# Kernel optimization log

Measured on AMD Instinct MI355X. Metric: run time of the kernel, lower is better.

Reference implementation:

```python
import jax, jax.numpy as jnp
import numpy as np

H = 768        # hidden_size
NH = 12        # num_attention_heads
HD = H // NH   # head dim = 64
FF = 4 * H     # intermediate_size = 3072
EPS = 1e-12


def setup_inputs() -> dict:
    key = jax.random.key(0)
    ks = jax.random.split(key, 16)
    s = 0.02
    return {
        "hidden_state": jax.random.normal(ks[0], (16, 512, H), dtype=jnp.float32),
        "Wq": jax.random.normal(ks[1], (H, H), dtype=jnp.float32) * s,
        "bq": jnp.zeros((H,), jnp.float32),
        "Wk": jax.random.normal(ks[2], (H, H), dtype=jnp.float32) * s,
        "bk": jnp.zeros((H,), jnp.float32),
        "Wv": jax.random.normal(ks[3], (H, H), dtype=jnp.float32) * s,
        "bv": jnp.zeros((H,), jnp.float32),
        "Wo": jax.random.normal(ks[4], (H, H), dtype=jnp.float32) * s,
        "bo": jnp.zeros((H,), jnp.float32),
        "ln1_g": jnp.ones((H,), jnp.float32),
        "ln1_b": jnp.zeros((H,), jnp.float32),
        "W1": jax.random.normal(ks[5], (H, FF), dtype=jnp.float32) * s,
        "b1": jnp.zeros((FF,), jnp.float32),
        "W2": jax.random.normal(ks[6], (FF, H), dtype=jnp.float32) * s,
        "b2": jnp.zeros((H,), jnp.float32),
        "ln2_g": jnp.ones((H,), jnp.float32),
        "ln2_b": jnp.zeros((H,), jnp.float32),
    }


def _layer_norm(x, g, b):
    mu = jnp.mean(x, axis=-1, keepdims=True)
    var = jnp.mean(jnp.square(x - mu), axis=-1, keepdims=True)
    return (x - mu) * jax.lax.rsqrt(var + EPS) * g + b


def _split_heads(x):  # [b,s,H] -> [b,nh,s,hd]
    b, s, _ = x.shape
    return x.reshape(b, s, NH, HD).transpose(0, 2, 1, 3)


def reference(hidden_state, Wq, bq, Wk, bk, Wv, bv, Wo, bo,
              ln1_g, ln1_b, W1, b1, W2, b2, ln2_g, ln2_b):
    x = hidden_state
    b, s, _ = x.shape
    q = _split_heads(x @ Wq + bq)
    k = _split_heads(x @ Wk + bk)
    v = _split_heads(x @ Wv + bv)
    score = jnp.einsum("bhqd,bhkd->bhqk", q, k) / jnp.sqrt(jnp.float32(HD))
    score = jax.nn.softmax(score, axis=-1)  # dropout = identity (eval mode)
    ctx = jnp.einsum("bhqk,bhkd->bhqd", score, v)
    ctx = ctx.transpose(0, 2, 1, 3).reshape(b, s, H)
    attn_out = ctx @ Wo + bo
    h = _layer_norm(attn_out + x, ln1_g, ln1_b)
    ffn = jax.nn.gelu(h @ W1 + b1, approximate=False) @ W2 + b2
    return _layer_norm(ffn + h, ln2_g, ln2_b)
```

## Files before the change

### kernel.cpp

```cpp
#include <hip/hip_runtime.h>

typedef short short8 __attribute__((ext_vector_type(8)));
typedef float floatx4 __attribute__((ext_vector_type(4)));
typedef unsigned short u16;
typedef unsigned int u32;

__device__ __forceinline__ float bits2f(u16 u) {
  union { unsigned int i; float f; } w;
  w.i = ((unsigned int)u) << 16;
  return w.f;
}

__device__ __forceinline__ u16 f2bf(float f) {
  union { float f; unsigned int i; } w;
  w.f = f;
  unsigned int x = w.i;
  unsigned int r = (x + 0x7FFFu + ((x >> 16) & 1u)) >> 16;
  return (u16)r;
}

__device__ __forceinline__ void g2l16(const u16* g, u16* l) {
  __builtin_amdgcn_global_load_lds(
      (const __attribute__((address_space(1))) u32*)(const void*)g,
      (__attribute__((address_space(3))) u32*)(void*)l, 16, 0, 0);
}

__global__ __launch_bounds__(256) void prep_kernel(
    const float* __restrict__ x, u16* __restrict__ xb,
    const float* __restrict__ bq, const float* __restrict__ bk,
    const float* __restrict__ bv, float* __restrict__ biasqkv,
    const float* __restrict__ Wq, const float* __restrict__ Wk,
    const float* __restrict__ Wv, const float* __restrict__ Wo,
    const float* __restrict__ W1,
    u16* __restrict__ WTqkv, u16* __restrict__ WTo, u16* __restrict__ WT1) {
  __shared__ float tile[32][33];
  int bid = blockIdx.x;
  int tid = threadIdx.x;
  if (bid < 3072) {
    int i = bid * 256 + tid;
    const float4* p = (const float4*)x + (size_t)i * 2;
    float4 a = p[0], b = p[1];
    u16 t[8] = {f2bf(a.x), f2bf(a.y), f2bf(a.z), f2bf(a.w),
                f2bf(b.x), f2bf(b.y), f2bf(b.z), f2bf(b.w)};
    *(int4*)(xb + (size_t)i * 8) = *(const int4*)t;
    return;
  }
  if (bid < 3081) {
    int i = (bid - 3072) * 256 + tid;
    biasqkv[i] = (i < 768) ? bq[i] : (i < 1536 ? bk[i - 768] : bv[i - 1536]);
    return;
  }
  const float* W;
  u16* WT;
  int K, N, bx, by;
  if (bid < 5385) {
    int s = bid - 3081;
    int wsel = s / 576;
    int r = s - wsel * 576;
    K = 768; N = 768; bx = r % 24; by = r / 24;
    if (wsel == 0)      { W = Wq; WT = WTqkv; }
    else if (wsel == 1) { W = Wk; WT = WTqkv + 768 * 768; }
    else if (wsel == 2) { W = Wv; WT = WTqkv + 2 * 768 * 768; }
    else                { W = Wo; WT = WTo; }
  } else {
    int r = bid - 5385;
    K = 768; N = 3072; bx = r % 96; by = r / 96;
    W = W1; WT = WT1;
  }
  int tx = tid & 31, ty = tid >> 5;
  int n0 = bx * 32, k0 = by * 32;
#pragma unroll
  for (int i = 0; i < 4; i++)
    tile[ty + i * 8][tx] = W[(size_t)(k0 + ty + i * 8) * N + n0 + tx];
  __syncthreads();
#pragma unroll
  for (int i = 0; i < 4; i++)
    WT[(size_t)(n0 + ty + i * 8) * K + k0 + tx] = f2bf(tile[tx][ty + i * 8]);
}

__global__ __launch_bounds__(256) void transpose_k(const float* __restrict__ W,
                                                   u16* __restrict__ WT,
                                                   int K, int N) {
  __shared__ float tile[32][33];
  int tx = threadIdx.x & 31;
  int ty = threadIdx.x >> 5;
  int n0 = blockIdx.x * 32;
  int k0 = blockIdx.y * 32;
#pragma unroll
  for (int i = 0; i < 4; i++)
    tile[ty + i * 8][tx] = W[(size_t)(k0 + ty + i * 8) * N + n0 + tx];
  __syncthreads();
#pragma unroll
  for (int i = 0; i < 4; i++)
    WT[(size_t)(n0 + ty + i * 8) * K + k0 + tx] = f2bf(tile[tx][ty + i * 8]);
}

template <int BN>
__global__ __launch_bounds__(256) void gemm_m97(
    const u16* __restrict__ A, int lda, const u16* __restrict__ BT,
    const float* __restrict__ bias, void* __restrict__ Cv,
    int M, int N, int K, int act, int c_fp32) {
  constexpr int BM = 128, BK = 32;
  __shared__ __align__(16) u16 As[BM * BK];
  __shared__ __align__(16) u16 Bs[BN * BK];
  int tid = threadIdx.x;
  int wave = tid >> 6;
  int lane = tid & 63;
  int l15 = lane & 15;
  int quad = lane >> 4;

  int nb = gridDim.x;
  int lin = blockIdx.y * nb + blockIdx.x;
  int xcd = lin & 7;
  int i = lin >> 3;
  int grp = i / 48;
  int rem = i - grp * 48;
  int nblk = grp * 6 + (rem % 6);
  int mblk = (xcd << 3) + rem / 6;
  int m0 = mblk * BM;
  int n0 = nblk * BN;

  constexpr int MT = (BN == 128) ? 4 : 2;
  constexpr int NT = 4;
  int wm = (BN == 128) ? (wave & 1) * 64 : wave * 32;
  int wn = (BN == 128) ? (wave >> 1) * 64 : 0;

  floatx4 acc[MT][NT];
#pragma unroll
  for (int mi = 0; mi < MT; mi++)
#pragma unroll
    for (int ni = 0; ni < NT; ni++) acc[mi][ni] = (floatx4){0.f, 0.f, 0.f, 0.f};

  int srow = tid >> 2;
  int scol = (tid & 3) * 8;
  const u16* Ag0 = A + (size_t)(m0 + srow) * lda + scol;
  const u16* Ag1 = A + (size_t)(m0 + 64 + srow) * lda + scol;
  const u16* Bg0 = BT + (size_t)(n0 + srow) * K + scol;
  u16* AsW0 = As + wave * 512;
  u16* AsW1 = As + 2048 + wave * 512;
  u16* BsW0 = Bs + wave * 512;

  for (int k0 = 0; k0 < K; k0 += BK) {
    g2l16(Ag0 + k0, AsW0);
    g2l16(Ag1 + k0, AsW1);
    g2l16(Bg0 + k0, BsW0);
    if constexpr (BN == 128) {
      const u16* Bg1 = BT + (size_t)(n0 + 64 + srow) * K + scol;
      g2l16(Bg1 + k0, Bs + 2048 + wave * 512);
    }
    __syncthreads();
    short8 af[MT], bfr[NT];
#pragma unroll
    for (int mi = 0; mi < MT; mi++)
      af[mi] = *(const short8*)&As[(wm + mi * 16 + l15) * BK + quad * 8];
#pragma unroll
    for (int ni = 0; ni < NT; ni++)
      bfr[ni] = *(const short8*)&Bs[(wn + ni * 16 + l15) * BK + quad * 8];
#pragma unroll
    for (int mi = 0; mi < MT; mi++)
#pragma unroll
      for (int ni = 0; ni < NT; ni++)
        acc[mi][ni] = __builtin_amdgcn_mfma_f32_16x16x32_bf16(
            af[mi], bfr[ni], acc[mi][ni], 0, 0, 0);
    __syncthreads();
  }

#pragma unroll
  for (int mi = 0; mi < MT; mi++) {
#pragma unroll
    for (int ni = 0; ni < NT; ni++) {
      int col = n0 + wn + ni * 16 + l15;
      float bv = bias[col];
#pragma unroll
      for (int r = 0; r < 4; r++) {
        int row = m0 + wm + mi * 16 + quad * 4 + r;
        float v = acc[mi][ni][r] + bv;
        if (act == 1) v = 0.5f * v * (1.0f + erff(v * 0.70710678118654752f));
        if (c_fp32) ((float*)Cv)[(size_t)row * N + col] = v;
        else        ((u16*)Cv)[(size_t)row * N + col] = f2bf(v);
      }
    }
  }
}

__global__ __launch_bounds__(256) void attn_kernel(u16* __restrict__ qkv) {
  __shared__ __align__(16) u16 Qs[64][72];
  __shared__ __align__(16) u16 Ks[64][72];
  __shared__ __align__(16) u16 Vt[64][72];
  __shared__ __align__(16) u16 Ps[4][16][72];

  const int LD = 2304;
  int bh = blockIdx.x;
  int b = bh / 12;
  int h = bh - b * 12;
  int q0 = blockIdx.y * 64;
  size_t base = (size_t)b * 512 * LD + (size_t)h * 64;
  const u16* qg = qkv + base;
  const u16* kg = qkv + base + 768;
  const u16* vg = qkv + base + 1536;
  int tid = threadIdx.x;
  int wave = tid >> 6;
  int lane = tid & 63;
  int l15 = lane & 15;
  int quad = lane >> 4;

  int srow = tid >> 2;
  int sd = (tid & 3) * 16;

  {
    const u16* qp = qg + (size_t)(q0 + srow) * LD + sd;
    *(int4*)&Qs[srow][sd]     = *(const int4*)qp;
    *(int4*)&Qs[srow][sd + 8] = *(const int4*)(qp + 8);
  }
  __syncthreads();

  short8 aQ[2];
#pragma unroll
  for (int k = 0; k < 2; k++)
    aQ[k] = *(const short8*)&Qs[16 * wave + l15][k * 32 + quad * 8];

  floatx4 O[4];
  float m_r[4], l_r[4];
#pragma unroll
  for (int nt = 0; nt < 4; nt++) O[nt] = (floatx4){0.f, 0.f, 0.f, 0.f};
#pragma unroll
  for (int r = 0; r < 4; r++) { m_r[r] = -1e30f; l_r[r] = 0.f; }

  const float cst = 0.18033688011112042f;

  for (int c = 0; c < 8; c++) {
    const u16* kp = kg + (size_t)(c * 64 + srow) * LD + sd;
    const u16* vp = vg + (size_t)(c * 64 + srow) * LD + sd;
    int4 kv0 = *(const int4*)kp;
    int4 kv1 = *(const int4*)(kp + 8);
    int4 vv0 = *(const int4*)vp;
    int4 vv1 = *(const int4*)(vp + 8);
    __syncthreads();
    *(int4*)&Ks[srow][sd]     = kv0;
    *(int4*)&Ks[srow][sd + 8] = kv1;
    {
      u16 tv[16];
      *(int4*)tv = vv0;
      *(int4*)(tv + 8) = vv1;
#pragma unroll
      for (int j = 0; j < 16; j++) Vt[sd + j][srow] = tv[j];
    }
    __syncthreads();

    floatx4 S[4];
#pragma unroll
    for (int nt = 0; nt < 4; nt++) {
      floatx4 s = {0.f, 0.f, 0.f, 0.f};
      short8 bK0 = *(const short8*)&Ks[nt * 16 + l15][quad * 8];
      short8 bK1 = *(const short8*)&Ks[nt * 16 + l15][32 + quad * 8];
      s = __builtin_amdgcn_mfma_f32_16x16x32_bf16(aQ[0], bK0, s, 0, 0, 0);
      s = __builtin_amdgcn_mfma_f32_16x16x32_bf16(aQ[1], bK1, s, 0, 0, 0);
      S[nt] = s;
    }

#pragma unroll
    for (int r = 0; r < 4; r++) {
      float s0 = S[0][r] * cst, s1 = S[1][r] * cst;
      float s2 = S[2][r] * cst, s3 = S[3][r] * cst;
      float mr = fmaxf(fmaxf(s0, s1), fmaxf(s2, s3));
#pragma unroll
      for (int off = 1; off < 16; off <<= 1) mr = fmaxf(mr, __shfl_xor(mr, off, 16));
      float m_new = fmaxf(m_r[r], mr);
      float alpha = exp2f(m_r[r] - m_new);
      m_r[r] = m_new;
      float p0 = exp2f(s0 - m_new), p1 = exp2f(s1 - m_new);
      float p2 = exp2f(s2 - m_new), p3 = exp2f(s3 - m_new);
      S[0][r] = p0; S[1][r] = p1; S[2][r] = p2; S[3][r] = p3;
      float sum = p0 + p1 + p2 + p3;
#pragma unroll
      for (int off = 1; off < 16; off <<= 1) sum += __shfl_xor(sum, off, 16);
      l_r[r] = l_r[r] * alpha + sum;
      O[0][r] *= alpha; O[1][r] *= alpha; O[2][r] *= alpha; O[3][r] *= alpha;
    }

#pragma unroll
    for (int nt = 0; nt < 4; nt++)
#pragma unroll
      for (int r = 0; r < 4; r++)
        Ps[wave][quad * 4 + r][nt * 16 + l15] = f2bf(S[nt][r]);

    short8 aP[2];
#pragma unroll
    for (int k = 0; k < 2; k++)
      aP[k] = *(const short8*)&Ps[wave][l15][k * 32 + quad * 8];

#pragma unroll
    for (int nt = 0; nt < 4; nt++) {
      short8 bV0 = *(const short8*)&Vt[nt * 16 + l15][quad * 8];
      short8 bV1 = *(const short8*)&Vt[nt * 16 + l15][32 + quad * 8];
      O[nt] = __builtin_amdgcn_mfma_f32_16x16x32_bf16(aP[0], bV0, O[nt], 0, 0, 0);
      O[nt] = __builtin_amdgcn_mfma_f32_16x16x32_bf16(aP[1], bV1, O[nt], 0, 0, 0);
    }
  }

#pragma unroll
  for (int r = 0; r < 4; r++) {
    float inv = 1.0f / l_r[r];
    int row = q0 + 16 * wave + quad * 4 + r;
    u16* cp = qkv + base + (size_t)row * LD;
#pragma unroll
    for (int nt = 0; nt < 4; nt++)
      cp[nt * 16 + l15] = f2bf(O[nt][r] * inv);
  }
}

__global__ __launch_bounds__(256) void ln1_kernel(
    const u16* __restrict__ a, const float* __restrict__ r,
    const float* __restrict__ g, const float* __restrict__ bb,
    u16* __restrict__ out) {
  int row = blockIdx.x;
  int tid = threadIdx.x;
  __shared__ float red[4];
  const u16* ap = a + (size_t)row * 768;
  const float* rp = r + (size_t)row * 768;
  float x0 = bits2f(ap[tid]) + rp[tid];
  float x1 = bits2f(ap[tid + 256]) + rp[tid + 256];
  float x2 = bits2f(ap[tid + 512]) + rp[tid + 512];
  float s = x0 + x1 + x2;
#pragma unroll
  for (int off = 32; off > 0; off >>= 1) s += __shfl_xor(s, off, 64);
  if ((tid & 63) == 0) red[tid >> 6] = s;
  __syncthreads();
  float mu = (red[0] + red[1] + red[2] + red[3]) * (1.0f / 768.0f);
  float d0 = x0 - mu, d1 = x1 - mu, d2 = x2 - mu;
  float vs = d0 * d0 + d1 * d1 + d2 * d2;
#pragma unroll
  for (int off = 32; off > 0; off >>= 1) vs += __shfl_xor(vs, off, 64);
  __syncthreads();
  if ((tid & 63) == 0) red[tid >> 6] = vs;
  __syncthreads();
  float var = (red[0] + red[1] + red[2] + red[3]) * (1.0f / 768.0f);
  float rstd = rsqrtf(var + 1e-12f);
  size_t o = (size_t)row * 768;
  out[o + tid]       = f2bf(d0 * rstd * g[tid] + bb[tid]);
  out[o + tid + 256] = f2bf(d1 * rstd * g[tid + 256] + bb[tid + 256]);
  out[o + tid + 512] = f2bf(d2 * rstd * g[tid + 512] + bb[tid + 512]);
}

__global__ __launch_bounds__(256) void ln2_kernel(
    const float* __restrict__ a, const u16* __restrict__ r,
    const float* __restrict__ g, const float* __restrict__ bb,
    float* __restrict__ out) {
  int row = blockIdx.x;
  int tid = threadIdx.x;
  __shared__ float red[4];
  const float* ap = a + (size_t)row * 768;
  const u16* rp = r + (size_t)row * 768;
  float x0 = ap[tid] + bits2f(rp[tid]);
  float x1 = ap[tid + 256] + bits2f(rp[tid + 256]);
  float x2 = ap[tid + 512] + bits2f(rp[tid + 512]);
  float s = x0 + x1 + x2;
#pragma unroll
  for (int off = 32; off > 0; off >>= 1) s += __shfl_xor(s, off, 64);
  if ((tid & 63) == 0) red[tid >> 6] = s;
  __syncthreads();
  float mu = (red[0] + red[1] + red[2] + red[3]) * (1.0f / 768.0f);
  float d0 = x0 - mu, d1 = x1 - mu, d2 = x2 - mu;
  float vs = d0 * d0 + d1 * d1 + d2 * d2;
#pragma unroll
  for (int off = 32; off > 0; off >>= 1) vs += __shfl_xor(vs, off, 64);
  __syncthreads();
  if ((tid & 63) == 0) red[tid >> 6] = vs;
  __syncthreads();
  float var = (red[0] + red[1] + red[2] + red[3]) * (1.0f / 768.0f);
  float rstd = rsqrtf(var + 1e-12f);
  size_t o = (size_t)row * 768;
  out[o + tid]       = d0 * rstd * g[tid] + bb[tid];
  out[o + tid + 256] = d1 * rstd * g[tid + 256] + bb[tid + 256];
  out[o + tid + 512] = d2 * rstd * g[tid + 512] + bb[tid + 512];
}

extern "C" void kernel_launch(void* const* d_in, const int* in_sizes, int n_in,
                              void* d_out, int out_size, void* d_ws, size_t ws_size,
                              hipStream_t stream) {
  (void)in_sizes; (void)n_in; (void)out_size; (void)ws_size;
  const float* x    = (const float*)d_in[0];
  const float* Wq   = (const float*)d_in[1];
  const float* bq   = (const float*)d_in[2];
  const float* Wk   = (const float*)d_in[3];
  const float* bk   = (const float*)d_in[4];
  const float* Wv   = (const float*)d_in[5];
  const float* bv   = (const float*)d_in[6];
  const float* Wo   = (const float*)d_in[7];
  const float* bo   = (const float*)d_in[8];
  const float* ln1g = (const float*)d_in[9];
  const float* ln1b = (const float*)d_in[10];
  const float* W1   = (const float*)d_in[11];
  const float* b1   = (const float*)d_in[12];
  const float* W2   = (const float*)d_in[13];
  const float* b2   = (const float*)d_in[14];
  const float* ln2g = (const float*)d_in[15];
  const float* ln2b = (const float*)d_in[16];

  const int M = 16 * 512, H = 768, FF = 3072;
  const size_t MH = (size_t)M * H;
  const size_t HH = (size_t)H * H;

  u16* ws    = (u16*)d_ws;
  u16* qkv   = ws;
  u16* xb    = ws + 3 * MH;
  u16* aob   = xb;
  u16* ffn1  = ws;
  u16* hb    = ws + 4 * MH;
  u16* WTqkv = ws + 5 * MH;
  u16* WTo   = WTqkv + 3 * HH;
  u16* WT1   = WTqkv + 4 * HH;
  u16* WT2   = WTqkv;
  float* biasqkv = (float*)(WT1 + 4 * HH);
  float* outf = (float*)d_out;

  dim3 tb(256);
  prep_kernel<<<dim3(7689), tb, 0, stream>>>(x, xb, bq, bk, bv, biasqkv,
                                             Wq, Wk, Wv, Wo, W1,
                                             WTqkv, WTo, WT1);

  gemm_m97<128><<<dim3(2304 / 128, M / 128), tb, 0, stream>>>(
      xb, H, WTqkv, biasqkv, qkv, M, 2304, H, 0, 0);

  attn_kernel<<<dim3(192, 8), tb, 0, stream>>>(qkv);

  gemm_m97<64><<<dim3(H / 64, M / 128), tb, 0, stream>>>(
      qkv, 2304, WTo, bo, aob, M, H, H, 0, 0);
  ln1_kernel<<<dim3(M), tb, 0, stream>>>(aob, x, ln1g, ln1b, hb);

  transpose_k<<<dim3(H / 32, FF / 32), tb, 0, stream>>>(W2, WT2, FF, H);

  gemm_m97<128><<<dim3(FF / 128, M / 128), tb, 0, stream>>>(
      hb, H, WT1, b1, ffn1, M, FF, H, 1, 0);
  gemm_m97<64><<<dim3(H / 64, M / 128), tb, 0, stream>>>(
      ffn1, FF, WT2, b2, outf, M, H, FF, 0, 1);
  ln2_kernel<<<dim3(M), tb, 0, stream>>>(outf, hb, ln2g, ln2b, outf);
}
```

Before: 411.3 us.

## Double-buffer GEMM LDS tiles and use tanh-form GELU approximation

The GEMM kernel now keeps two LDS buffers for the A and B tiles. It issues the global-to-LDS load for the next K-step before computing on the current one, and drops the trailing barrier so there is one barrier per iteration. The goal is to overlap global memory latency with the MFMA work. Separately, the exact erf-based GELU in the epilogue is replaced by a sigmoid/tanh-style approximation using __expf, which is cheaper but deviates slightly from the exact GELU the reference specifies. Doubling the LDS footprint may reduce how many blocks fit on each CU.

```diff
diff --git a/kernel.cpp b/kernel.cpp
--- a/kernel.cpp
+++ b/kernel.cpp
@@ -17,6 +17,11 @@
   unsigned int x = w.i;
   unsigned int r = (x + 0x7FFFu + ((x >> 16) & 1u)) >> 16;
   return (u16)r;
+}
+
+__device__ __forceinline__ float gelu_f(float x) {
+  float t = x * (1.5957691216057308f + 0.07135481283247914f * x * x);
+  return x / (1.0f + __expf(-t));
 }
 
 __device__ __forceinline__ void g2l16(const u16* g, u16* l) {
@@ -101,8 +106,9 @@
     const float* __restrict__ bias, void* __restrict__ Cv,
     int M, int N, int K, int act, int c_fp32) {
   constexpr int BM = 128, BK = 32;
-  __shared__ __align__(16) u16 As[BM * BK];
-  __shared__ __align__(16) u16 Bs[BN * BK];
+  constexpr int ASZ = BM * BK, BSZ = BN * BK;
+  __shared__ __align__(16) u16 As[2 * ASZ];
+  __shared__ __align__(16) u16 Bs[2 * BSZ];
   int tid = threadIdx.x;
   int wave = tid >> 6;
   int lane = tid & 63;
@@ -136,33 +142,39 @@
   const u16* Ag0 = A + (size_t)(m0 + srow) * lda + scol;
   const u16* Ag1 = A + (size_t)(m0 + 64 + srow) * lda + scol;
   const u16* Bg0 = BT + (size_t)(n0 + srow) * K + scol;
-  u16* AsW0 = As + wave * 512;
-  u16* AsW1 = As + 2048 + wave * 512;
-  u16* BsW0 = Bs + wave * 512;
-
-  for (int k0 = 0; k0 < K; k0 += BK) {
-    g2l16(Ag0 + k0, AsW0);
-    g2l16(Ag1 + k0, AsW1);
-    g2l16(Bg0 + k0, BsW0);
-    if constexpr (BN == 128) {
-      const u16* Bg1 = BT + (size_t)(n0 + 64 + srow) * K + scol;
-      g2l16(Bg1 + k0, Bs + 2048 + wave * 512);
-    }
+  const u16* Bg1 = BT + (size_t)(n0 + 64 + srow) * K + scol;
+  int woff = wave * 512;
+
+  auto stage = [&](int k0, int buf) {
+    u16* Ab = As + buf * ASZ;
+    u16* Bb = Bs + buf * BSZ;
+    g2l16(Ag0 + k0, Ab + woff);
+    g2l16(Ag1 + k0, Ab + 2048 + woff);
+    g2l16(Bg0 + k0, Bb + woff);
+    if constexpr (BN == 128) g2l16(Bg1 + k0, Bb + 2048 + woff);
+  };
+
+  int nk = K / BK;
+  stage(0, 0);
+  for (int k = 0; k < nk; k++) {
+    int cur = k & 1;
     __syncthreads();
+    if (k + 1 < nk) stage((k + 1) * BK, cur ^ 1);
+    const u16* Ab = As + cur * ASZ;
+    const u16* Bb = Bs + cur * BSZ;
     short8 af[MT], bfr[NT];
 #pragma unroll
     for (int mi = 0; mi < MT; mi++)
-      af[mi] = *(const short8*)&As[(wm + mi * 16 + l15) * BK + quad * 8];
+      af[mi] = *(const short8*)&Ab[(wm + mi * 16 + l15) * BK + quad * 8];
 #pragma unroll
     for (int ni = 0; ni < NT; ni++)
-      bfr[ni] = *(const short8*)&Bs[(wn + ni * 16 + l15) * BK + quad * 8];
+      bfr[ni] = *(const short8*)&Bb[(wn + ni * 16 + l15) * BK + quad * 8];
 #pragma unroll
     for (int mi = 0; mi < MT; mi++)
 #pragma unroll
       for (int ni = 0; ni < NT; ni++)
         acc[mi][ni] = __builtin_amdgcn_mfma_f32_16x16x32_bf16(
             af[mi], bfr[ni], acc[mi][ni], 0, 0, 0);
-    __syncthreads();
   }
 
 #pragma unroll
@@ -175,7 +187,7 @@
       for (int r = 0; r < 4; r++) {
         int row = m0 + wm + mi * 16 + quad * 4 + r;
         float v = acc[mi][ni][r] + bv;
-        if (act == 1) v = 0.5f * v * (1.0f + erff(v * 0.70710678118654752f));
+        if (act == 1) v = gelu_f(v);
         if (c_fp32) ((float*)Cv)[(size_t)row * N + col] = v;
         else        ((u16*)Cv)[(size_t)row * N + col] = f2bf(v);
       }
```

Result: faster. 398.5 us (-3.1%).
